# Optimization experiments

Hardware: AMD Instinct MI355X
Metric: run time of the kernel (lower is better)

Reference implementation:

```python
import jax, jax.numpy as jnp
import numpy as np
import math

N_NODES = 50000
N_EDGES = 800000
NFEAT = 512
NHID = 128
NCLASS = 128
NLAYERS = 16
LAMDA = 0.5
ALPHA = 0.1


def setup_inputs() -> dict:
    key = jax.random.key(0)
    k1, k2, k3, k4, k5, k6, k7, k8 = jax.random.split(key, 8)
    x = jax.random.normal(k1, (N_NODES, NFEAT), dtype=jnp.float32)
    # edges with no self loops: col = (row + offset) % N, offset in [1, N)
    row = jax.random.randint(k2, (N_EDGES,), 0, N_NODES, dtype=jnp.int32)
    off = jax.random.randint(k3, (N_EDGES,), 1, N_NODES, dtype=jnp.int32)
    col = (row + off) % N_NODES
    edge_idx = jnp.stack([row, col], axis=0)
    # conv weights: uniform(-stdv, stdv), stdv = 1/sqrt(out_features)
    stdv = 1.0 / math.sqrt(NHID)
    conv_w = jax.random.uniform(k4, (NLAYERS, NHID, NHID), jnp.float32, -stdv, stdv)
    # fc layers (stored as [in, out]; equivalent to torch Linear y = x @ W.T + b)
    fc0_w = jax.random.normal(k5, (NFEAT, NHID), jnp.float32) * (1.0 / math.sqrt(NFEAT))
    fc0_b = jax.random.normal(k6, (NHID,), jnp.float32) * 0.01
    fc1_w = jax.random.normal(k7, (NHID, NCLASS), jnp.float32) * (1.0 / math.sqrt(NHID))
    fc1_b = jax.random.normal(k8, (NCLASS,), jnp.float32) * 0.01
    return {"x": x, "edge_idx": edge_idx, "conv_w": conv_w,
            "fc0_w": fc0_w, "fc0_b": fc0_b, "fc1_w": fc1_w, "fc1_b": fc1_b}


def reference(x, edge_idx, conv_w, fc0_w, fc0_b, fc1_w, fc1_b):
    # eval mode: dropout is identity
    n = x.shape[0]
    loop = jnp.arange(n, dtype=edge_idx.dtype)
    # add_remaining_self_loops: inputs have no self loops -> append unit loops
    row = jnp.concatenate([edge_idx[0], loop])
    col = jnp.concatenate([edge_idx[1], loop])
    w = jnp.ones(row.shape[0], dtype=x.dtype)
    # symmetric normalization: D^-1/2 A D^-1/2
    deg = jax.ops.segment_sum(w, row, num_segments=n)
    dinv = jnp.where(deg > 0, jax.lax.rsqrt(deg), 0.0).astype(x.dtype)
    w = dinv[row] * w * dinv[col]

    h0 = jax.nn.relu(x @ fc0_w + fc0_b)  # [N, NHID]
    thetas = jnp.log(LAMDA / jnp.arange(1, NLAYERS + 1, dtype=x.dtype) + 1.0)

    def layer(h, wt):
        Wl, theta = wt
        # SpMM: hi[r] = sum_{(r,c) in E} w_rc * h[c]
        hi = jax.ops.segment_sum(w[:, None] * h[col], row, num_segments=n)
        support = (1.0 - ALPHA) * hi + ALPHA * h0
        out = theta * (support @ Wl) + (1.0 - theta) * support
        return jax.nn.relu(out), None

    h, _ = jax.lax.scan(layer, h0, (conv_w, thetas))
    return h @ fc1_w + fc1_b  # [N, NCLASS]
```

## Files before the change

### kernel.cpp

```cpp
#include <hip/hip_runtime.h>
#include <hip/hip_bf16.h>
#include <math.h>

#define N_NODES_C 50000
#define N_EDGES_C 800000
#define NFEAT_C 512
#define NH_C 128
#define NLAYERS_C 16
#define LDB 136

typedef __attribute__((ext_vector_type(8))) short short8;
typedef __attribute__((ext_vector_type(4))) float f32x4;

__device__ __forceinline__ float b2f(unsigned short h) {
    union { unsigned int u; float f; } v; v.u = ((unsigned int)h) << 16; return v.f;
}
__device__ __forceinline__ unsigned short f2b(float f) {
    union { float f; unsigned int u; } v; v.f = f;
    unsigned int r = (v.u + 0x7fffu + ((v.u >> 16) & 1u)) >> 16;
    return (unsigned short)r;
}


__global__ __launch_bounds__(256) void k_count(const int* __restrict__ row,
                                               int* __restrict__ cnt) {
    int e = blockIdx.x * 256 + threadIdx.x;
    atomicAdd(&cnt[row[e]], 1);
}

__global__ __launch_bounds__(256) void k_scan1(const int* __restrict__ cnt,
                                               int* __restrict__ locex,
                                               int* __restrict__ partials, int n) {
    __shared__ int sm[256];
    int t = threadIdx.x;
    int i = blockIdx.x * 256 + t;
    int v = (i < n) ? cnt[i] : 0;
    sm[t] = v;
    __syncthreads();
    for (int o = 1; o < 256; o <<= 1) {
        int x = (t >= o) ? sm[t - o] : 0;
        __syncthreads();
        sm[t] += x;
        __syncthreads();
    }
    if (i < n) locex[i] = sm[t] - v;
    if (t == 255) partials[blockIdx.x] = sm[255];
}

__global__ __launch_bounds__(256) void k_scan2(int* __restrict__ partials, int np) {
    __shared__ int sm[256];
    int t = threadIdx.x;
    int v = (t < np) ? partials[t] : 0;
    sm[t] = v;
    __syncthreads();
    for (int o = 1; o < 256; o <<= 1) {
        int x = (t >= o) ? sm[t - o] : 0;
        __syncthreads();
        sm[t] += x;
        __syncthreads();
    }
    if (t < np) partials[t] = sm[t] - v;
}

__global__ __launch_bounds__(256) void k_scan3(const int* __restrict__ cnt,
                                               const int* __restrict__ locex,
                                               const int* __restrict__ partials,
                                               int* __restrict__ rowptr,
                                               int* __restrict__ cursor,
                                               float* __restrict__ dinv,
                                               int n, int ne) {
    int i = blockIdx.x * 256 + threadIdx.x;
    if (i < n) {
        int rp = locex[i] + partials[i >> 8];
        rowptr[i] = rp;
        cursor[i] = rp;
        dinv[i] = 1.0f / sqrtf((float)(cnt[i] + 1));
    }
    if (i == 0) rowptr[n] = ne;
}

__global__ __launch_bounds__(256) void k_fill(const int* __restrict__ row,
                                              const int* __restrict__ col,
                                              int* __restrict__ cursor,
                                              int* __restrict__ colsorted) {
    int e = blockIdx.x * 256 + threadIdx.x;
    int p = atomicAdd(&cursor[row[e]], 1);
    colsorted[p] = col[e];
}


__global__ __launch_bounds__(256) void k_convt128(const float* __restrict__ src,
                                                  unsigned short* __restrict__ dst,
                                                  int total) {
    int i = blockIdx.x * 256 + threadIdx.x;
    if (i >= total) return;
    int l = i >> 14, w = i & 16383;
    int n = w >> 7, k = w & 127;
    dst[i] = f2b(src[(l << 14) + (k << 7) + n]);
}

__global__ __launch_bounds__(256) void k_convt_fc0(const float* __restrict__ src,
                                                   unsigned short* __restrict__ dst) {
    int i = blockIdx.x * 256 + threadIdx.x;
    int n = i >> 9, k = i & 511;
    dst[i] = f2b(src[(k << 7) + n]);
}


__global__ __launch_bounds__(256) void k_spmm(const unsigned short* __restrict__ hs,
                                              const unsigned short* __restrict__ h0,
                                              const float* __restrict__ dinv,
                                              const int* __restrict__ rowptr,
                                              const int* __restrict__ cols,
                                              unsigned short* __restrict__ sout) {
    const int w = threadIdx.x >> 6, ln = threadIdx.x & 63;
    const int r = blockIdx.x * 4 + w;
    const unsigned int* hsu = (const unsigned int*)hs;
    unsigned int su = hsu[(size_t)r * 64 + ln];
    unsigned int hu = ((const unsigned int*)h0)[(size_t)r * 64 + ln];
    float dr = 0.9f * dinv[r];
    int e = rowptr[r];
    const int end = rowptr[r + 1];

    float a0 = b2f((unsigned short)(su & 0xffffu));
    float a1 = b2f((unsigned short)(su >> 16));
    float b0 = 0.f, b1 = 0.f;
    for (; e + 3 < end; e += 4) {
        int c0 = cols[e], c1 = cols[e + 1], c2 = cols[e + 2], c3 = cols[e + 3];
        unsigned int u0 = hsu[(size_t)c0 * 64 + ln];
        unsigned int u1 = hsu[(size_t)c1 * 64 + ln];
        unsigned int u2 = hsu[(size_t)c2 * 64 + ln];
        unsigned int u3 = hsu[(size_t)c3 * 64 + ln];
        a0 += b2f((unsigned short)(u0 & 0xffffu)) + b2f((unsigned short)(u1 & 0xffffu));
        a1 += b2f((unsigned short)(u0 >> 16)) + b2f((unsigned short)(u1 >> 16));
        b0 += b2f((unsigned short)(u2 & 0xffffu)) + b2f((unsigned short)(u3 & 0xffffu));
        b1 += b2f((unsigned short)(u2 >> 16)) + b2f((unsigned short)(u3 >> 16));
    }
    for (; e < end; e++) {
        int c = cols[e];
        unsigned int u = hsu[(size_t)c * 64 + ln];
        a0 += b2f((unsigned short)(u & 0xffffu));
        a1 += b2f((unsigned short)(u >> 16));
    }
    a0 += b0;
    a1 += b1;
    float s0 = dr * a0 + 0.1f * b2f((unsigned short)(hu & 0xffffu));
    float s1 = dr * a1 + 0.1f * b2f((unsigned short)(hu >> 16));
    ((unsigned int*)sout)[(size_t)r * 64 + ln] =
        (unsigned int)f2b(s0) | ((unsigned int)f2b(s1) << 16);
}


__global__ __launch_bounds__(256) void k_gemm_blend(
    const unsigned short* __restrict__ S, const float* __restrict__ dinv,
    const unsigned short* __restrict__ WT, unsigned short* __restrict__ hdst,
    float theta, int use_dinv) {
    __shared__ __align__(16) unsigned short s_lds[64 * LDB];
    __shared__ __align__(16) unsigned short bt[128 * LDB];
    const int tid = threadIdx.x;
    const int w = tid >> 6, ln = tid & 63;
    const int quad = ln >> 4, l16 = ln & 15;
    const int block_base = blockIdx.x * 64;

    for (int chunk = tid; chunk < 128 * 16; chunk += 256) {
        int n = chunk >> 4, k8 = (chunk & 15) << 3;
        *(short8*)&bt[n * LDB + k8] = *(const short8*)&WT[(n << 7) + k8];
    }
    for (int chunk = tid; chunk < 64 * 16; chunk += 256) {
        int n = chunk >> 4, k8 = (chunk & 15) << 3;
        int row = block_base + n;
        short8 v = {};
        if (row < N_NODES_C) v = *(const short8*)&S[(size_t)row * NH_C + k8];
        *(short8*)&s_lds[n * LDB + k8] = v;
    }
    __syncthreads();

    f32x4 acc[8];
#pragma unroll
    for (int j = 0; j < 8; j++) acc[j] = (f32x4){0.f, 0.f, 0.f, 0.f};
#pragma unroll
    for (int ki = 0; ki < 128; ki += 32) {
        short8 af = *(const short8*)&s_lds[((w << 4) + l16) * LDB + ki + quad * 8];
#pragma unroll
        for (int nt = 0; nt < 8; nt++) {
            short8 bf = *(const short8*)&bt[(nt * 16 + l16) * LDB + ki + quad * 8];
            acc[nt] = __builtin_amdgcn_mfma_f32_16x16x32_bf16(af, bf, acc[nt], 0, 0, 0);
        }
    }

#pragma unroll
    for (int reg = 0; reg < 4; reg++) {
        int lr = (w << 4) + (quad << 2) + reg;
        int r = block_base + lr;
        float drv = dinv[(r < N_NODES_C) ? r : (N_NODES_C - 1)];
#pragma unroll
        for (int nt = 0; nt < 8; nt++) {
            int n = nt * 16 + l16;
            float s = b2f(s_lds[lr * LDB + n]);
            float v = theta * acc[nt][reg] + (1.f - theta) * s;
            v = fmaxf(v, 0.f);
            if (use_dinv) v *= drv;
            s_lds[lr * LDB + n] = f2b(v);
        }
    }
    __syncthreads();
    for (int chunk = tid; chunk < 64 * 16; chunk += 256) {
        int lr = chunk >> 4, c8 = (chunk & 15) << 3;
        int row = block_base + lr;
        if (row < N_NODES_C)
            *(short8*)&hdst[(size_t)row * NH_C + c8] = *(const short8*)&s_lds[lr * LDB + c8];
    }
}


template <int AFP32, int MT>
__global__ __launch_bounds__(256) void k_gemm(
    const void* __restrict__ Av, const unsigned short* __restrict__ WT,
    int M, int K,
    const float* __restrict__ bias, const float* __restrict__ dinv,
    unsigned short* __restrict__ out0, unsigned short* __restrict__ out1,
    float* __restrict__ outf, int mode) {
    __shared__ __align__(16) unsigned short bt[128 * LDB];
    const int tid = threadIdx.x;
    const int w = tid >> 6, ln = tid & 63;
    const int quad = ln >> 4, l16 = ln & 15;
    const int ROWS = 64 * MT;
    const int block_base = blockIdx.x * ROWS;
    const int m_base = block_base + w * (16 * MT);

    f32x4 acc[MT][8];
#pragma unroll
    for (int i = 0; i < MT; i++)
#pragma unroll
        for (int j = 0; j < 8; j++) acc[i][j] = (f32x4){0.f, 0.f, 0.f, 0.f};

    for (int kc = 0; kc < K; kc += 128) {
        for (int chunk = tid; chunk < 128 * 16; chunk += 256) {
            int n = chunk >> 4, k8 = (chunk & 15) << 3;
            *(short8*)&bt[n * LDB + k8] = *(const short8*)&WT[(size_t)n * K + kc + k8];
        }
        __syncthreads();
#pragma unroll
        for (int ki = 0; ki < 128; ki += 32) {
            short8 bf[8];
#pragma unroll
            for (int nt = 0; nt < 8; nt++)
                bf[nt] = *(const short8*)&bt[(nt * 16 + l16) * LDB + ki + quad * 8];
#pragma unroll
            for (int mt = 0; mt < MT; mt++) {
                int row = m_base + mt * 16 + l16;
                if (row >= M) row = M - 1;
                short8 af;
                if (AFP32) {
                    const float* A = (const float*)Av;
                    const float* p = &A[(size_t)row * K + kc + ki + quad * 8];
                    float4 f0 = *(const float4*)p;
                    float4 f1 = *(const float4*)(p + 4);
                    af[0] = (short)f2b(f0.x); af[1] = (short)f2b(f0.y);
                    af[2] = (short)f2b(f0.z); af[3] = (short)f2b(f0.w);
                    af[4] = (short)f2b(f1.x); af[5] = (short)f2b(f1.y);
                    af[6] = (short)f2b(f1.z); af[7] = (short)f2b(f1.w);
                } else {
                    const unsigned short* A = (const unsigned short*)Av;
                    af = *(const short8*)&A[(size_t)row * K + kc + ki + quad * 8];
                }
#pragma unroll
                for (int nt = 0; nt < 8; nt++)
                    acc[mt][nt] = __builtin_amdgcn_mfma_f32_16x16x32_bf16(
                        af, bf[nt], acc[mt][nt], 0, 0, 0);
            }
        }
        __syncthreads();
    }

    if (mode == 2) {
#pragma unroll
        for (int mt = 0; mt < MT; mt++)
#pragma unroll
            for (int reg = 0; reg < 4; reg++) {
                int r = m_base + mt * 16 + quad * 4 + reg;
                if (r >= M) continue;
#pragma unroll
                for (int nt = 0; nt < 8; nt++) {
                    int n = nt * 16 + l16;
                    outf[(size_t)r * NH_C + n] = acc[mt][nt][reg] + bias[n];
                }
            }
        return;
    }

#pragma unroll
    for (int mt = 0; mt < MT; mt++)
#pragma unroll
        for (int reg = 0; reg < 4; reg++) {
            int lr = w * (16 * MT) + mt * 16 + quad * 4 + reg;
#pragma unroll
            for (int nt = 0; nt < 8; nt++) {
                int n = nt * 16 + l16;
                float v = acc[mt][nt][reg] + bias[n];
                bt[lr * LDB + n] = f2b(fmaxf(v, 0.f));
            }
        }
    __syncthreads();
    for (int chunk = tid; chunk < ROWS * 16; chunk += 256) {
        int lr = chunk >> 4, c8 = (chunk & 15) << 3;
        int row = block_base + lr;
        if (row >= M) continue;
        short8 v = *(const short8*)&bt[lr * LDB + c8];
        *(short8*)&out1[(size_t)row * NH_C + c8] = v;
        float dr = dinv[row];
        short8 o;
#pragma unroll
        for (int j = 0; j < 8; j++)
            o[j] = (short)f2b(b2f((unsigned short)v[j]) * dr);
        *(short8*)&out0[(size_t)row * NH_C + c8] = o;
    }
}


extern "C" void kernel_launch(void* const* d_in, const int* in_sizes, int n_in,
                              void* d_out, int out_size, void* d_ws, size_t ws_size,
                              hipStream_t stream) {
    const float* x = (const float*)d_in[0];
    const int* edge = (const int*)d_in[1];
    const float* convw = (const float*)d_in[2];
    const float* fc0w = (const float*)d_in[3];
    const float* fc0b = (const float*)d_in[4];
    const float* fc1w = (const float*)d_in[5];
    const float* fc1b = (const float*)d_in[6];
    const int* erow = edge;
    const int* ecol = edge + N_EDGES_C;

    char* ws = (char*)d_ws;
    size_t off = 0;
    auto alloc = [&](size_t bytes) -> void* {
        off = (off + 255) & ~(size_t)255;
        void* p = ws + off;
        off += bytes;
        return p;
    };
    int* cnt = (int*)alloc(N_NODES_C * 4);
    int* cursor = (int*)alloc(N_NODES_C * 4);
    int* locex = (int*)alloc(N_NODES_C * 4);
    int* partials = (int*)alloc(1024);
    int* rowptr = (int*)alloc((N_NODES_C + 1) * 4);
    float* dinv = (float*)alloc(N_NODES_C * 4);
    int* colsorted = (int*)alloc(N_EDGES_C * 4);
    unsigned short* wconvT = (unsigned short*)alloc((size_t)NLAYERS_C * NH_C * NH_C * 2);
    unsigned short* wfc0T = (unsigned short*)alloc((size_t)NFEAT_C * NH_C * 2);
    unsigned short* wfc1T = (unsigned short*)alloc((size_t)NH_C * NH_C * 2);
    unsigned short* h0 = (unsigned short*)alloc((size_t)N_NODES_C * NH_C * 2);
    unsigned short* hsA = (unsigned short*)alloc((size_t)N_NODES_C * NH_C * 2);
    unsigned short* hsB = (unsigned short*)alloc((size_t)N_NODES_C * NH_C * 2);
    unsigned short* sbuf = (unsigned short*)alloc((size_t)N_NODES_C * NH_C * 2);
    (void)ws_size; (void)n_in; (void)in_sizes; (void)out_size;

    k_convt128<<<NLAYERS_C * NH_C * NH_C / 256, 256, 0, stream>>>(
        convw, wconvT, NLAYERS_C * NH_C * NH_C);
    k_convt_fc0<<<NFEAT_C * NH_C / 256, 256, 0, stream>>>(fc0w, wfc0T);
    k_convt128<<<NH_C * NH_C / 256, 256, 0, stream>>>(fc1w, wfc1T, NH_C * NH_C);

    hipMemsetAsync(cnt, 0, N_NODES_C * 4, stream);
    k_count<<<N_EDGES_C / 256, 256, 0, stream>>>(erow, cnt);
    const int NB = (N_NODES_C + 255) / 256;
    k_scan1<<<NB, 256, 0, stream>>>(cnt, locex, partials, N_NODES_C);
    k_scan2<<<1, 256, 0, stream>>>(partials, NB);
    k_scan3<<<NB, 256, 0, stream>>>(cnt, locex, partials, rowptr, cursor, dinv,
                                    N_NODES_C, N_EDGES_C);
    k_fill<<<N_EDGES_C / 256, 256, 0, stream>>>(erow, ecol, cursor, colsorted);

    const int GB1 = (N_NODES_C + 63) / 64;
    k_gemm<1, 1><<<GB1, 256, 0, stream>>>(x, wfc0T, N_NODES_C, NFEAT_C, fc0b, dinv,
                                          hsA, h0, nullptr, 0);
    unsigned short* cur = hsA;
    unsigned short* nxt = hsB;
    for (int l = 0; l < NLAYERS_C; l++) {
        k_spmm<<<N_NODES_C / 4, 256, 0, stream>>>(cur, h0, dinv, rowptr, colsorted,
                                                  sbuf);
        float theta = logf(0.5f / (float)(l + 1) + 1.0f);
        k_gemm_blend<<<GB1, 256, 0, stream>>>(sbuf, dinv,
                                              wconvT + (size_t)l * NH_C * NH_C, nxt,
                                              theta, (l < NLAYERS_C - 1) ? 1 : 0);
        unsigned short* t = cur; cur = nxt; nxt = t;
    }
    k_gemm<0, 1><<<GB1, 256, 0, stream>>>(cur, wfc1T, N_NODES_C, NH_C, fc1b, dinv,
                                          nullptr, nullptr, (float*)d_out, 2);
}
```

Baseline: 1.080 ms.

## Fuse SpMM aggregation with per-layer GEMM blend into one kernel

Merges the per-layer SpMM and the GEMM/blend kernel into one 512-thread kernel. Each block aggregates 32 rows into LDS, then eight waves split the 32x128 tile for MFMA and the blend. This removes the intermediate sbuf round trip and one launch per layer, but each block reloads the 128x128 weight tile for only 32 rows. The fc GEMM also now stages A tiles (fp32 converted to bf16) in LDS instead of loading fragments directly from global.

```diff
diff --git a/kernel.cpp b/kernel.cpp
--- a/kernel.cpp
+++ b/kernel.cpp
@@ -107,105 +107,103 @@
 }
 
 
-__global__ __launch_bounds__(256) void k_spmm(const unsigned short* __restrict__ hs,
-                                              const unsigned short* __restrict__ h0,
-                                              const float* __restrict__ dinv,
-                                              const int* __restrict__ rowptr,
-                                              const int* __restrict__ cols,
-                                              unsigned short* __restrict__ sout) {
-    const int w = threadIdx.x >> 6, ln = threadIdx.x & 63;
-    const int r = blockIdx.x * 4 + w;
-    const unsigned int* hsu = (const unsigned int*)hs;
-    unsigned int su = hsu[(size_t)r * 64 + ln];
-    unsigned int hu = ((const unsigned int*)h0)[(size_t)r * 64 + ln];
-    float dr = 0.9f * dinv[r];
-    int e = rowptr[r];
-    const int end = rowptr[r + 1];
-
-    float a0 = b2f((unsigned short)(su & 0xffffu));
-    float a1 = b2f((unsigned short)(su >> 16));
-    float b0 = 0.f, b1 = 0.f;
-    for (; e + 3 < end; e += 4) {
-        int c0 = cols[e], c1 = cols[e + 1], c2 = cols[e + 2], c3 = cols[e + 3];
-        unsigned int u0 = hsu[(size_t)c0 * 64 + ln];
-        unsigned int u1 = hsu[(size_t)c1 * 64 + ln];
-        unsigned int u2 = hsu[(size_t)c2 * 64 + ln];
-        unsigned int u3 = hsu[(size_t)c3 * 64 + ln];
-        a0 += b2f((unsigned short)(u0 & 0xffffu)) + b2f((unsigned short)(u1 & 0xffffu));
-        a1 += b2f((unsigned short)(u0 >> 16)) + b2f((unsigned short)(u1 >> 16));
-        b0 += b2f((unsigned short)(u2 & 0xffffu)) + b2f((unsigned short)(u3 & 0xffffu));
-        b1 += b2f((unsigned short)(u2 >> 16)) + b2f((unsigned short)(u3 >> 16));
-    }
-    for (; e < end; e++) {
-        int c = cols[e];
-        unsigned int u = hsu[(size_t)c * 64 + ln];
-        a0 += b2f((unsigned short)(u & 0xffffu));
-        a1 += b2f((unsigned short)(u >> 16));
-    }
-    a0 += b0;
-    a1 += b1;
-    float s0 = dr * a0 + 0.1f * b2f((unsigned short)(hu & 0xffffu));
-    float s1 = dr * a1 + 0.1f * b2f((unsigned short)(hu >> 16));
-    ((unsigned int*)sout)[(size_t)r * 64 + ln] =
-        (unsigned int)f2b(s0) | ((unsigned int)f2b(s1) << 16);
-}
-
-
-__global__ __launch_bounds__(256) void k_gemm_blend(
-    const unsigned short* __restrict__ S, const float* __restrict__ dinv,
-    const unsigned short* __restrict__ WT, unsigned short* __restrict__ hdst,
-    float theta, int use_dinv) {
-    __shared__ __align__(16) unsigned short s_lds[64 * LDB];
+__global__ __launch_bounds__(512) void k_layer(
+    const unsigned short* __restrict__ hs, const unsigned short* __restrict__ h0,
+    const float* __restrict__ dinv, const int* __restrict__ rowptr,
+    const int* __restrict__ cols, const unsigned short* __restrict__ WT,
+    unsigned short* __restrict__ hdst, float theta, int use_dinv) {
+    __shared__ __align__(16) unsigned short s_lds[32 * LDB];
     __shared__ __align__(16) unsigned short bt[128 * LDB];
     const int tid = threadIdx.x;
     const int w = tid >> 6, ln = tid & 63;
     const int quad = ln >> 4, l16 = ln & 15;
-    const int block_base = blockIdx.x * 64;
-
-    for (int chunk = tid; chunk < 128 * 16; chunk += 256) {
+    const int block_base = blockIdx.x * 32;
+
+    for (int chunk = tid; chunk < 128 * 16; chunk += 512) {
         int n = chunk >> 4, k8 = (chunk & 15) << 3;
         *(short8*)&bt[n * LDB + k8] = *(const short8*)&WT[(n << 7) + k8];
     }
-    for (int chunk = tid; chunk < 64 * 16; chunk += 256) {
-        int n = chunk >> 4, k8 = (chunk & 15) << 3;
-        int row = block_base + n;
-        short8 v = {};
-        if (row < N_NODES_C) v = *(const short8*)&S[(size_t)row * NH_C + k8];
-        *(short8*)&s_lds[n * LDB + k8] = v;
-    }
-    __syncthreads();
-
-    f32x4 acc[8];
-#pragma unroll
-    for (int j = 0; j < 8; j++) acc[j] = (f32x4){0.f, 0.f, 0.f, 0.f};
+
+    const unsigned int* hsu = (const unsigned int*)hs;
+    const unsigned int* h0u = (const unsigned int*)h0;
+#pragma unroll
+    for (int i = 0; i < 4; i++) {
+        const int lr = (w << 2) + i;
+        const int r = block_base + lr;
+        unsigned int* srow = (unsigned int*)&s_lds[lr * LDB];
+        if (r >= N_NODES_C) { srow[ln] = 0; continue; }
+        unsigned int su = hsu[(size_t)r * 64 + ln];
+        unsigned int hu = h0u[(size_t)r * 64 + ln];
+        float dr = 0.9f * dinv[r];
+        int e = rowptr[r];
+        const int end = rowptr[r + 1];
+        float a0 = b2f((unsigned short)(su & 0xffffu));
+        float a1 = b2f((unsigned short)(su >> 16));
+        float b0 = 0.f, b1 = 0.f;
+        for (; e + 3 < end; e += 4) {
+            int c0 = cols[e], c1 = cols[e + 1], c2 = cols[e + 2], c3 = cols[e + 3];
+            unsigned int u0 = hsu[(size_t)c0 * 64 + ln];
+            unsigned int u1 = hsu[(size_t)c1 * 64 + ln];
+            unsigned int u2 = hsu[(size_t)c2 * 64 + ln];
+            unsigned int u3 = hsu[(size_t)c3 * 64 + ln];
+            a0 += b2f((unsigned short)(u0 & 0xffffu)) + b2f((unsigned short)(u1 & 0xffffu));
+            a1 += b2f((unsigned short)(u0 >> 16)) + b2f((unsigned short)(u1 >> 16));
+            b0 += b2f((unsigned short)(u2 & 0xffffu)) + b2f((unsigned short)(u3 & 0xffffu));
+            b1 += b2f((unsigned short)(u2 >> 16)) + b2f((unsigned short)(u3 >> 16));
+        }
+        for (; e < end; e++) {
+            int c = cols[e];
+            unsigned int u = hsu[(size_t)c * 64 + ln];
+            a0 += b2f((unsigned short)(u & 0xffffu));
+            a1 += b2f((unsigned short)(u >> 16));
+        }
+        a0 += b0;
+        a1 += b1;
+        float s0 = dr * a0 + 0.1f * b2f((unsigned short)(hu & 0xffffu));
+        float s1 = dr * a1 + 0.1f * b2f((unsigned short)(hu >> 16));
+        srow[ln] = (unsigned int)f2b(s0) | ((unsigned int)f2b(s1) << 16);
+    }
+    __syncthreads();
+
+    const int rt = w >> 2;
+    const int ct0 = (w & 3) << 1;
+    f32x4 acc0 = (f32x4){0.f, 0.f, 0.f, 0.f};
+    f32x4 acc1 = (f32x4){0.f, 0.f, 0.f, 0.f};
 #pragma unroll
     for (int ki = 0; ki < 128; ki += 32) {
-        short8 af = *(const short8*)&s_lds[((w << 4) + l16) * LDB + ki + quad * 8];
-#pragma unroll
-        for (int nt = 0; nt < 8; nt++) {
-            short8 bf = *(const short8*)&bt[(nt * 16 + l16) * LDB + ki + quad * 8];
-            acc[nt] = __builtin_amdgcn_mfma_f32_16x16x32_bf16(af, bf, acc[nt], 0, 0, 0);
-        }
-    }
+        short8 af = *(const short8*)&s_lds[((rt << 4) + l16) * LDB + ki + quad * 8];
+        short8 bf0 = *(const short8*)&bt[((ct0 << 4) + l16) * LDB + ki + quad * 8];
+        short8 bf1 = *(const short8*)&bt[(((ct0 + 1) << 4) + l16) * LDB + ki + quad * 8];
+        acc0 = __builtin_amdgcn_mfma_f32_16x16x32_bf16(af, bf0, acc0, 0, 0, 0);
+        acc1 = __builtin_amdgcn_mfma_f32_16x16x32_bf16(af, bf1, acc1, 0, 0, 0);
+    }
+    __syncthreads();
 
 #pragma unroll
     for (int reg = 0; reg < 4; reg++) {
-        int lr = (w << 4) + (quad << 2) + reg;
+        int lr = (rt << 4) + (quad << 2) + reg;
         int r = block_base + lr;
         float drv = dinv[(r < N_NODES_C) ? r : (N_NODES_C - 1)];
-#pragma unroll
-        for (int nt = 0; nt < 8; nt++) {
-            int n = nt * 16 + l16;
+        {
+            int n = (ct0 << 4) + l16;
             float s = b2f(s_lds[lr * LDB + n]);
-            float v = theta * acc[nt][reg] + (1.f - theta) * s;
+            float v = theta * acc0[reg] + (1.f - theta) * s;
             v = fmaxf(v, 0.f);
             if (use_dinv) v *= drv;
             s_lds[lr * LDB + n] = f2b(v);
         }
-    }
-    __syncthreads();
-    for (int chunk = tid; chunk < 64 * 16; chunk += 256) {
-        int lr = chunk >> 4, c8 = (chunk & 15) << 3;
+        {
+            int n = ((ct0 + 1) << 4) + l16;
+            float s = b2f(s_lds[lr * LDB + n]);
+            float v = theta * acc1[reg] + (1.f - theta) * s;
+            v = fmaxf(v, 0.f);
+            if (use_dinv) v *= drv;
+            s_lds[lr * LDB + n] = f2b(v);
+        }
+    }
+    __syncthreads();
+    {
+        int lr = tid >> 4, c8 = (tid & 15) << 3;
         int row = block_base + lr;
         if (row < N_NODES_C)
             *(short8*)&hdst[(size_t)row * NH_C + c8] = *(const short8*)&s_lds[lr * LDB + c8];
@@ -213,7 +211,7 @@
 }
 
 
-template <int AFP32, int MT>
+template <int AFP32>
 __global__ __launch_bounds__(256) void k_gemm(
     const void* __restrict__ Av, const unsigned short* __restrict__ WT,
     int M, int K,
@@ -221,53 +219,53 @@
     unsigned short* __restrict__ out0, unsigned short* __restrict__ out1,
     float* __restrict__ outf, int mode) {
     __shared__ __align__(16) unsigned short bt[128 * LDB];
+    __shared__ __align__(16) unsigned short at[64 * LDB];
     const int tid = threadIdx.x;
     const int w = tid >> 6, ln = tid & 63;
     const int quad = ln >> 4, l16 = ln & 15;
-    const int ROWS = 64 * MT;
-    const int block_base = blockIdx.x * ROWS;
-    const int m_base = block_base + w * (16 * MT);
-
-    f32x4 acc[MT][8];
-#pragma unroll
-    for (int i = 0; i < MT; i++)
-#pragma unroll
-        for (int j = 0; j < 8; j++) acc[i][j] = (f32x4){0.f, 0.f, 0.f, 0.f};
+    const int block_base = blockIdx.x * 64;
+    const int m_base = block_base + w * 16;
+
+    f32x4 acc[8];
+#pragma unroll
+    for (int j = 0; j < 8; j++) acc[j] = (f32x4){0.f, 0.f, 0.f, 0.f};
 
     for (int kc = 0; kc < K; kc += 128) {
         for (int chunk = tid; chunk < 128 * 16; chunk += 256) {
             int n = chunk >> 4, k8 = (chunk & 15) << 3;
             *(short8*)&bt[n * LDB + k8] = *(const short8*)&WT[(size_t)n * K + kc + k8];
         }
+        if (AFP32) {
+            const float* A = (const float*)Av;
+            for (int chunk = tid; chunk < 64 * 32; chunk += 256) {
+                int row = chunk >> 5, c4 = (chunk & 31) << 2;
+                int r = block_base + row;
+                if (r >= M) r = M - 1;
+                float4 f = *(const float4*)&A[(size_t)r * K + kc + c4];
+                unsigned long long pk =
+                    (unsigned long long)f2b(f.x) |
+                    ((unsigned long long)f2b(f.y) << 16) |
+                    ((unsigned long long)f2b(f.z) << 32) |
+                    ((unsigned long long)f2b(f.w) << 48);
+                *(unsigned long long*)&at[row * LDB + c4] = pk;
+            }
+        } else {
+            const unsigned short* A = (const unsigned short*)Av;
+            for (int chunk = tid; chunk < 64 * 16; chunk += 256) {
+                int row = chunk >> 4, k8 = (chunk & 15) << 3;
+                int r = block_base + row;
+                if (r >= M) r = M - 1;
+                *(short8*)&at[row * LDB + k8] = *(const short8*)&A[(size_t)r * K + kc + k8];
+            }
+        }
         __syncthreads();
 #pragma unroll
         for (int ki = 0; ki < 128; ki += 32) {
-            short8 bf[8];
-#pragma unroll
-            for (int nt = 0; nt < 8; nt++)
-                bf[nt] = *(const short8*)&bt[(nt * 16 + l16) * LDB + ki + quad * 8];
-#pragma unroll
-            for (int mt = 0; mt < MT; mt++) {
-                int row = m_base + mt * 16 + l16;
-                if (row >= M) row = M - 1;
-                short8 af;
-                if (AFP32) {
-                    const float* A = (const float*)Av;
-                    const float* p = &A[(size_t)row * K + kc + ki + quad * 8];
-                    float4 f0 = *(const float4*)p;
-                    float4 f1 = *(const float4*)(p + 4);
-                    af[0] = (short)f2b(f0.x); af[1] = (short)f2b(f0.y);
-                    af[2] = (short)f2b(f0.z); af[3] = (short)f2b(f0.w);
-                    af[4] = (short)f2b(f1.x); af[5] = (short)f2b(f1.y);
-                    af[6] = (short)f2b(f1.z); af[7] = (short)f2b(f1.w);
-                } else {
-                    const unsigned short* A = (const unsigned short*)Av;
-                    af = *(const short8*)&A[(size_t)row * K + kc + ki + quad * 8];
-                }
-#pragma unroll
-                for (int nt = 0; nt < 8; nt++)
-                    acc[mt][nt] = __builtin_amdgcn_mfma_f32_16x16x32_bf16(
-                        af, bf[nt], acc[mt][nt], 0, 0, 0);
+            short8 af = *(const short8*)&at[((w << 4) + l16) * LDB + ki + quad * 8];
+#pragma unroll
+            for (int nt = 0; nt < 8; nt++) {
+                short8 bf = *(const short8*)&bt[(nt * 16 + l16) * LDB + ki + quad * 8];
+                acc[nt] = __builtin_amdgcn_mfma_f32_16x16x32_bf16(af, bf, acc[nt], 0, 0, 0);
             }
         }
         __syncthreads();
@@ -275,34 +273,30 @@
 
     if (mode == 2) {
 #pragma unroll
-        for (int mt = 0; mt < MT; mt++)
-#pragma unroll
-            for (int reg = 0; reg < 4; reg++) {
-                int r = m_base + mt * 16 + quad * 4 + reg;
-                if (r >= M) continue;
-#pragma unroll
-                for (int nt = 0; nt < 8; nt++) {
-                    int n = nt * 16 + l16;
-                    outf[(size_t)r * NH_C + n] = acc[mt][nt][reg] + bias[n];
-                }
-            }
-        return;
-    }
-
-#pragma unroll
-    for (int mt = 0; mt < MT; mt++)
-#pragma unroll
         for (int reg = 0; reg < 4; reg++) {
-            int lr = w * (16 * MT) + mt * 16 + quad * 4 + reg;
+            int r = m_base + quad * 4 + reg;
+            if (r >= M) continue;
 #pragma unroll
             for (int nt = 0; nt < 8; nt++) {
                 int n = nt * 16 + l16;
-                float v = acc[mt][nt][reg] + bias[n];
-                bt[lr * LDB + n] = f2b(fmaxf(v, 0.f));
+                outf[(size_t)r * NH_C + n] = acc[nt][reg] + bias[n];
             }
         }
-    __syncthreads();
-    for (int chunk = tid; chunk < ROWS * 16; chunk += 256) {
+        return;
+    }
+
+#pragma unroll
+    for (int reg = 0; reg < 4; reg++) {
+        int lr = w * 16 + quad * 4 + reg;
+#pragma unroll
+        for (int nt = 0; nt < 8; nt++) {
+            int n = nt * 16 + l16;
+            float v = acc[nt][reg] + bias[n];
+            bt[lr * LDB + n] = f2b(fmaxf(v, 0.f));
+        }
+    }
+    __syncthreads();
+    for (int chunk = tid; chunk < 64 * 16; chunk += 256) {
         int lr = chunk >> 4, c8 = (chunk & 15) << 3;
         int row = block_base + lr;
         if (row >= M) continue;
@@ -352,7 +346,6 @@
     unsigned short* h0 = (unsigned short*)alloc((size_t)N_NODES_C * NH_C * 2);
     unsigned short* hsA = (unsigned short*)alloc((size_t)N_NODES_C * NH_C * 2);
     unsigned short* hsB = (unsigned short*)alloc((size_t)N_NODES_C * NH_C * 2);
-    unsigned short* sbuf = (unsigned short*)alloc((size_t)N_NODES_C * NH_C * 2);
     (void)ws_size; (void)n_in; (void)in_sizes; (void)out_size;
 
     k_convt128<<<NLAYERS_C * NH_C * NH_C / 256, 256, 0, stream>>>(
@@ -370,19 +363,18 @@
     k_fill<<<N_EDGES_C / 256, 256, 0, stream>>>(erow, ecol, cursor, colsorted);
 
     const int GB1 = (N_NODES_C + 63) / 64;
-    k_gemm<1, 1><<<GB1, 256, 0, stream>>>(x, wfc0T, N_NODES_C, NFEAT_C, fc0b, dinv,
-                                          hsA, h0, nullptr, 0);
+    const int GBL = (N_NODES_C + 31) / 32;
+    k_gemm<1><<<GB1, 256, 0, stream>>>(x, wfc0T, N_NODES_C, NFEAT_C, fc0b, dinv,
+                                       hsA, h0, nullptr, 0);
     unsigned short* cur = hsA;
     unsigned short* nxt = hsB;
     for (int l = 0; l < NLAYERS_C; l++) {
-        k_spmm<<<N_NODES_C / 4, 256, 0, stream>>>(cur, h0, dinv, rowptr, colsorted,
-                                                  sbuf);
         float theta = logf(0.5f / (float)(l + 1) + 1.0f);
-        k_gemm_blend<<<GB1, 256, 0, stream>>>(sbuf, dinv,
-                                              wconvT + (size_t)l * NH_C * NH_C, nxt,
-                                              theta, (l < NLAYERS_C - 1) ? 1 : 0);
+        k_layer<<<GBL, 512, 0, stream>>>(cur, h0, dinv, rowptr, colsorted,
+                                         wconvT + (size_t)l * NH_C * NH_C, nxt,
+                                         theta, (l < NLAYERS_C - 1) ? 1 : 0);
         unsigned short* t = cur; cur = nxt; nxt = t;
     }
-    k_gemm<0, 1><<<GB1, 256, 0, stream>>>(cur, wfc1T, N_NODES_C, NH_C, fc1b, dinv,
-                                          nullptr, nullptr, (float*)d_out, 2);
-}
+    k_gemm<0><<<GB1, 256, 0, stream>>>(cur, wfc1T, N_NODES_C, NH_C, fc1b, dinv,
+                                       nullptr, nullptr, (float*)d_out, 2);
+}
```

New measurement: 1.288 ms. 19.3% more time.

## Split SpMM wavefront into four edge groups with 16-byte row loads

Applied to the files above, without the earlier changes.

Each wavefront now handles one row as four 16-lane groups. Each group loads a full 256-byte neighbor row using uint4 per lane and processes a different edge, so four edges are in flight per instruction. Partial sums are then reduced across groups with xor shuffles. The aim is wider memory transactions and more gather parallelism per row, at the cost of shuffle reductions, more accumulator registers, and idle lanes on the tail.

```diff
diff --git a/kernel.cpp b/kernel.cpp
--- a/kernel.cpp
+++ b/kernel.cpp
@@ -107,6 +107,17 @@
 }
 
 
+__device__ __forceinline__ void acc8(float* a, uint4 u) {
+    a[0] += b2f((unsigned short)(u.x & 0xffffu));
+    a[1] += b2f((unsigned short)(u.x >> 16));
+    a[2] += b2f((unsigned short)(u.y & 0xffffu));
+    a[3] += b2f((unsigned short)(u.y >> 16));
+    a[4] += b2f((unsigned short)(u.z & 0xffffu));
+    a[5] += b2f((unsigned short)(u.z >> 16));
+    a[6] += b2f((unsigned short)(u.w & 0xffffu));
+    a[7] += b2f((unsigned short)(u.w >> 16));
+}
+
 __global__ __launch_bounds__(256) void k_spmm(const unsigned short* __restrict__ hs,
                                               const unsigned short* __restrict__ h0,
                                               const float* __restrict__ dinv,
@@ -115,39 +126,65 @@
                                               unsigned short* __restrict__ sout) {
     const int w = threadIdx.x >> 6, ln = threadIdx.x & 63;
     const int r = blockIdx.x * 4 + w;
-    const unsigned int* hsu = (const unsigned int*)hs;
-    unsigned int su = hsu[(size_t)r * 64 + ln];
-    unsigned int hu = ((const unsigned int*)h0)[(size_t)r * 64 + ln];
-    float dr = 0.9f * dinv[r];
+    const int g = ln >> 4, gi = ln & 15;
+    const uint4* hs4 = (const uint4*)hs;
+    const uint4* h04 = (const uint4*)h0;
+
+    float a[8];
+#pragma unroll
+    for (int j = 0; j < 8; j++) a[j] = 0.f;
+
     int e = rowptr[r];
     const int end = rowptr[r + 1];
 
-    float a0 = b2f((unsigned short)(su & 0xffffu));
-    float a1 = b2f((unsigned short)(su >> 16));
-    float b0 = 0.f, b1 = 0.f;
+    if (g == 0) {
+        uint4 u = hs4[(size_t)r * 16 + gi];
+        acc8(a, u);
+    }
+    for (; e + 15 < end; e += 16) {
+        int cA = cols[e + g];
+        int cB = cols[e + 4 + g];
+        int cC = cols[e + 8 + g];
+        int cD = cols[e + 12 + g];
+        uint4 uA = hs4[(size_t)cA * 16 + gi];
+        uint4 uB = hs4[(size_t)cB * 16 + gi];
+        uint4 uC = hs4[(size_t)cC * 16 + gi];
+        uint4 uD = hs4[(size_t)cD * 16 + gi];
+        acc8(a, uA);
+        acc8(a, uB);
+        acc8(a, uC);
+        acc8(a, uD);
+    }
     for (; e + 3 < end; e += 4) {
-        int c0 = cols[e], c1 = cols[e + 1], c2 = cols[e + 2], c3 = cols[e + 3];
-        unsigned int u0 = hsu[(size_t)c0 * 64 + ln];
-        unsigned int u1 = hsu[(size_t)c1 * 64 + ln];
-        unsigned int u2 = hsu[(size_t)c2 * 64 + ln];
-        unsigned int u3 = hsu[(size_t)c3 * 64 + ln];
-        a0 += b2f((unsigned short)(u0 & 0xffffu)) + b2f((unsigned short)(u1 & 0xffffu));
-        a1 += b2f((unsigned short)(u0 >> 16)) + b2f((unsigned short)(u1 >> 16));
-        b0 += b2f((unsigned short)(u2 & 0xffffu)) + b2f((unsigned short)(u3 & 0xffffu));
-        b1 += b2f((unsigned short)(u2 >> 16)) + b2f((unsigned short)(u3 >> 16));
-    }
-    for (; e < end; e++) {
-        int c = cols[e];
-        unsigned int u = hsu[(size_t)c * 64 + ln];
-        a0 += b2f((unsigned short)(u & 0xffffu));
-        a1 += b2f((unsigned short)(u >> 16));
-    }
-    a0 += b0;
-    a1 += b1;
-    float s0 = dr * a0 + 0.1f * b2f((unsigned short)(hu & 0xffffu));
-    float s1 = dr * a1 + 0.1f * b2f((unsigned short)(hu >> 16));
-    ((unsigned int*)sout)[(size_t)r * 64 + ln] =
-        (unsigned int)f2b(s0) | ((unsigned int)f2b(s1) << 16);
+        int c = cols[e + g];
+        uint4 u = hs4[(size_t)c * 16 + gi];
+        acc8(a, u);
+    }
+    int rem = end - e;
+    if (g < rem) {
+        int c = cols[e + g];
+        uint4 u = hs4[(size_t)c * 16 + gi];
+        acc8(a, u);
+    }
+
+#pragma unroll
+    for (int j = 0; j < 8; j++) {
+        a[j] += __shfl_xor(a[j], 16);
+        a[j] += __shfl_xor(a[j], 32);
+    }
+
+    float dr = 0.9f * dinv[r];
+    uint4 hv = h04[(size_t)r * 16 + gi];
+    uint4 o;
+    o.x = (unsigned int)f2b(dr * a[0] + 0.1f * b2f((unsigned short)(hv.x & 0xffffu))) |
+          ((unsigned int)f2b(dr * a[1] + 0.1f * b2f((unsigned short)(hv.x >> 16))) << 16);
+    o.y = (unsigned int)f2b(dr * a[2] + 0.1f * b2f((unsigned short)(hv.y & 0xffffu))) |
+          ((unsigned int)f2b(dr * a[3] + 0.1f * b2f((unsigned short)(hv.y >> 16))) << 16);
+    o.z = (unsigned int)f2b(dr * a[4] + 0.1f * b2f((unsigned short)(hv.z & 0xffffu))) |
+          ((unsigned int)f2b(dr * a[5] + 0.1f * b2f((unsigned short)(hv.z >> 16))) << 16);
+    o.w = (unsigned int)f2b(dr * a[6] + 0.1f * b2f((unsigned short)(hv.w & 0xffffu))) |
+          ((unsigned int)f2b(dr * a[7] + 0.1f * b2f((unsigned short)(hv.w >> 16))) << 16);
+    if (g == 0) ((uint4*)sout)[(size_t)r * 16 + gi] = o;
 }
 
 
```

Result: faster. 1.006 ms (-6.8%).
